# Kernel tuning notes

Measured on AMD Instinct MI355X. Metric: run time of the kernel, lower is better.

## Reference

```python
import jax, jax.numpy as jnp
import numpy as np

B, T, R, D, M = 4, 256, 100, 128, 256

def setup_inputs() -> dict:
    key = jax.random.key(0)
    ks = jax.random.split(key, 12)
    s = 0.02
    return {
        'x': jax.random.normal(ks[0], (B, T, R, D), dtype=jnp.float32),
        'mask': jax.random.randint(ks[1], (B, T), 0, 2).astype(jnp.int32),
        'Wq': jax.random.normal(ks[2], (D, D), dtype=jnp.float32) * s,
        'bq': jnp.zeros((D,), jnp.float32),
        'Wk': jax.random.normal(ks[3], (D, D), dtype=jnp.float32) * s,
        'bk': jnp.zeros((D,), jnp.float32),
        'Wv': jax.random.normal(ks[4], (D, D), dtype=jnp.float32) * s,
        'bv': jnp.zeros((D,), jnp.float32),
        'Wp': jax.random.normal(ks[5], (D, D), dtype=jnp.float32) * s,
        'bp': jnp.zeros((D,), jnp.float32),
        'ln_g': jnp.ones((D,), jnp.float32),
        'ln_b': jnp.zeros((D,), jnp.float32),
        'rel_table': jax.random.normal(ks[6], (2 * M - 1, 1), dtype=jnp.float32) * s,
    }


def reference(x, mask, Wq, bq, Wk, bk, Wv, bv, Wp, bp, ln_g, ln_b, rel_table):
    b, t, r, d = x.shape
    m = (rel_table.shape[0] + 1) // 2  # max_time_steps
    # faithful to torch .view(B*R, T, D): raw row-major reshape (no transpose)
    xr = x.reshape(b * r, t, d)
    q = xr @ Wq + bq
    k = xr @ Wk + bk
    v = xr @ Wv + bv
    scale = jnp.asarray(1.0 / np.sqrt(d), x.dtype)
    s = jnp.einsum('ntd,nsd->nts', q, k) * scale  # [B*R, T, T]
    # relative position bias
    ids = jnp.clip(jnp.arange(t)[:, None] - jnp.arange(t)[None, :] + (m - 1), 0, 2 * m - 2)
    s = s + rel_table[ids, 0][None, :, :]
    # padding mask (key and query sides)
    am = jnp.repeat(mask[:, None, :], r, axis=1).reshape(b * r, t)  # [B*R, T]
    neg = jnp.asarray(-1e9, s.dtype)
    s = jnp.where(am[:, None, :] == 0, neg, s)
    s = jnp.where(am[:, :, None] == 0, neg, s)
    # causal mask
    causal = jnp.triu(jnp.ones((t, t), dtype=bool), 1)
    s = jnp.where(causal[None, :, :], neg, s)
    w = jax.nn.softmax(s, axis=-1)
    ctx = jnp.einsum('nts,nsd->ntd', w, v)
    out = ctx @ Wp + bp
    y = xr + out
    mu = jnp.mean(y, axis=-1, keepdims=True)
    var = jnp.mean((y - mu) ** 2, axis=-1, keepdims=True)
    y = (y - mu) / jnp.sqrt(var + 1e-5) * ln_g + ln_b
    # faithful to torch .view(B, R, T, D).permute(0, 2, 1, 3)
    return y.reshape(b, r, t, d).transpose(0, 2, 1, 3)
```

## Files before the change

kernel.cpp:

```cpp
#include <hip/hip_runtime.h>
#include <hip/hip_bf16.h>
#include <stdint.h>

typedef float f32x4 __attribute__((ext_vector_type(4)));
typedef __bf16 bf16x8 __attribute__((ext_vector_type(8)));
typedef unsigned short u16;

#define MFMA16(a, b, c) __builtin_amdgcn_mfma_f32_16x16x32_bf16((a), (b), (c), 0, 0, 0)

__device__ __forceinline__ u16 f2bf(float f) {
  union { float f; uint32_t u; } v; v.f = f;
  uint32_t u = v.u;
  return (u16)((u + 0x7fffu + ((u >> 16) & 1u)) >> 16);
}
__device__ __forceinline__ float bf2f(u16 h) {
  union { uint32_t u; float f; } v; v.u = ((uint32_t)h) << 16;
  return v.f;
}

__global__ void prep_weights_kernel(const float* __restrict__ Wq, const float* __restrict__ Wk,
                                    const float* __restrict__ Wv, const float* __restrict__ Wp,
                                    u16* __restrict__ Wt) {
  int w = blockIdx.x;
  const float* W = (w == 0) ? Wq : (w == 1) ? Wk : (w == 2) ? Wv : Wp;
  int t = blockIdx.y * 256 + threadIdx.x;
  int c = t >> 7, k = t & 127;
  Wt[(w * 128 + c) * 128 + k] = f2bf(W[k * 128 + c]);
}

__global__ __launch_bounds__(512, 2) void fused11_kernel(
    const u16* __restrict__ Wt, const float* __restrict__ x,
    const int* __restrict__ mask, const float* __restrict__ rel,
    const float* __restrict__ bq, const float* __restrict__ bk,
    const float* __restrict__ bv, const float* __restrict__ bp,
    const float* __restrict__ ln_g, const float* __restrict__ ln_b,
    float* __restrict__ out) {
  __shared__ u16 KX[256][136];
  __shared__ u16 V_lds[128][264];
  __shared__ u16 P_lds[8][32][40];
  __shared__ float rel_lds[511];
  __shared__ float vmean_lds[128];
  const int tid = threadIdx.x;
  const int n = blockIdx.x;
  const int bb = n / 100, rr = n - bb * 100;
  const int* mrow = mask + bb * 256;
  if (tid < 511) rel_lds[tid] = rel[tid];
  const int l = tid & 63, wv = tid >> 6, l15 = l & 15, l4 = l >> 4;
  const int tt0 = wv * 32;

#define LOADW4(buf, ROWB)                                                  \
  do {                                                                     \
    const u16* _wp = Wt + (size_t)((ROWB) + l15) * 128 + l4 * 8;           \
    buf[0] = *(const bf16x8*)(_wp);                                        \
    buf[1] = *(const bf16x8*)(_wp + 32);                                   \
    buf[2] = *(const bf16x8*)(_wp + 64);                                   \
    buf[3] = *(const bf16x8*)(_wp + 96);                                   \
  } while (0)

  bf16x8 bA[4], bB[4];
  LOADW4(bA, 0);

  {
    int row = tt0 + (l >> 1), half = (l & 1) * 64;
    const float* src = x + ((size_t)(n * 256 + row)) * 128 + half;
    u16* dst = &KX[row][half];
    float4 xr[16];
#pragma unroll
    for (int j = 0; j < 16; ++j) xr[j] = ((const float4*)src)[j];
#pragma unroll
    for (int j = 0; j < 16; ++j) {
      dst[j * 4 + 0] = f2bf(xr[j].x); dst[j * 4 + 1] = f2bf(xr[j].y);
      dst[j * 4 + 2] = f2bf(xr[j].z); dst[j * 4 + 3] = f2bf(xr[j].w);
    }
  }
  int ttg[2][4], qm[2][4];
#pragma unroll
  for (int g = 0; g < 2; ++g)
#pragma unroll
    for (int rg = 0; rg < 4; ++rg) {
      ttg[g][rg] = tt0 + g * 16 + 4 * l4 + rg;
      qm[g][rg] = mrow[ttg[g][rg]];
    }

  bf16x8 af[2][4];
#pragma unroll
  for (int g = 0; g < 2; ++g)
#pragma unroll
    for (int ks = 0; ks < 4; ++ks)
      af[g][ks] = *(const bf16x8*)&KX[tt0 + g * 16 + l15][ks * 32 + l4 * 8];
  uint32_t xres[2][4][4];
#pragma unroll
  for (int g = 0; g < 2; ++g)
#pragma unroll
    for (int rg = 0; rg < 4; ++rg) {
      const u16* xr = &KX[tt0 + g * 16 + 4 * l4 + rg][0];
#pragma unroll
      for (int c = 0; c < 4; ++c)
        xres[g][rg][c] = (uint32_t)xr[c * 32 + l15] | ((uint32_t)xr[c * 32 + 16 + l15] << 16);
    }

  const float scale = 0.088388347648318447f;
  f32x4 t0, t1;
#define MF8(buf)                                                           \
  do {                                                                     \
    t0 = f32x4{0.f, 0.f, 0.f, 0.f}; t1 = f32x4{0.f, 0.f, 0.f, 0.f};       \
    _Pragma("unroll") for (int ks = 0; ks < 4; ++ks) {                     \
      t0 = MFMA16(af[0][ks], buf[ks], t0);                                 \
      t1 = MFMA16(af[1][ks], buf[ks], t1);                                 \
    }                                                                      \
  } while (0)

  bf16x8 qa[2][4];
#define QSTORE(CT)                                                         \
  do {                                                                     \
    float bqv = bq[(CT) * 16 + l15];                                       \
    _Pragma("unroll") for (int rg = 0; rg < 4; ++rg) {                     \
      P_lds[wv][4 * l4 + rg][((CT) & 1) * 16 + l15] = f2bf((t0[rg] + bqv) * scale); \
      P_lds[wv][16 + 4 * l4 + rg][((CT) & 1) * 16 + l15] = f2bf((t1[rg] + bqv) * scale); \
    }                                                                      \
    if ((CT) & 1) {                                                        \
      qa[0][(CT) >> 1] = *(const bf16x8*)&P_lds[wv][l15][l4 * 8];          \
      qa[1][(CT) >> 1] = *(const bf16x8*)&P_lds[wv][16 + l15][l4 * 8];     \
    }                                                                      \
  } while (0)
  LOADW4(bB, 16);
  MF8(bA); LOADW4(bA, 2 * 16);        QSTORE(0);
  MF8(bB); LOADW4(bB, 3 * 16);        QSTORE(1);
  MF8(bA); LOADW4(bA, 4 * 16);        QSTORE(2);
  MF8(bB); LOADW4(bB, 5 * 16);        QSTORE(3);
  MF8(bA); LOADW4(bA, 6 * 16);        QSTORE(4);
  MF8(bB); LOADW4(bB, 7 * 16);        QSTORE(5);
  MF8(bA); LOADW4(bA, 128 + wv * 16); QSTORE(6);
  MF8(bB); LOADW4(bB, 256 + wv * 16); QSTORE(7);

  __syncthreads();

  const float bkv = bk[wv * 16 + l15];
  const float bvv = bv[wv * 16 + l15];
  f32x4 kacc[16];
#pragma unroll
  for (int r = 0; r < 16; ++r) {
    bf16x8 xf[4];
#pragma unroll
    for (int ks = 0; ks < 4; ++ks)
      xf[ks] = *(const bf16x8*)&KX[r * 16 + l15][ks * 32 + l4 * 8];
    f32x4 ka = f32x4{0.f, 0.f, 0.f, 0.f};
    f32x4 va = f32x4{0.f, 0.f, 0.f, 0.f};
#pragma unroll
    for (int ks = 0; ks < 4; ++ks) {
      ka = MFMA16(xf[ks], bA[ks], ka);
      va = MFMA16(xf[ks], bB[ks], va);
    }
    kacc[r] = ka;
#pragma unroll
    for (int rg = 0; rg < 4; ++rg)
      V_lds[wv * 16 + l15][r * 16 + 4 * l4 + rg] = f2bf(va[rg] + bvv);
  }
  __syncthreads();
#pragma unroll
  for (int r = 0; r < 16; ++r)
#pragma unroll
    for (int rg = 0; rg < 4; ++rg)
      KX[r * 16 + 4 * l4 + rg][wv * 16 + l15] = f2bf(kacc[r][rg] + bkv);
  __syncthreads();

  {
    int d = tid >> 2, seg = tid & 3;
    const u16* vr = &V_lds[d][seg * 64];
    float s = 0.f;
#pragma unroll
    for (int j = 0; j < 8; ++j) {
      uint4 u = *(const uint4*)(vr + j * 8);
      s += bf2f((u16)(u.x & 0xffff)) + bf2f((u16)(u.x >> 16));
      s += bf2f((u16)(u.y & 0xffff)) + bf2f((u16)(u.y >> 16));
      s += bf2f((u16)(u.z & 0xffff)) + bf2f((u16)(u.z >> 16));
      s += bf2f((u16)(u.w & 0xffff)) + bf2f((u16)(u.w >> 16));
    }
    s += __shfl_xor(s, 1); s += __shfl_xor(s, 2);
    if (seg == 0) vmean_lds[d] = s * (1.f / 256.f);
  }
  float lsum[2][4]; f32x4 cacc[2][8];
#pragma unroll
  for (int g = 0; g < 2; ++g)
#pragma unroll
    for (int rg = 0; rg < 4; ++rg) lsum[g][rg] = 0.f;
#pragma unroll
  for (int g = 0; g < 2; ++g)
#pragma unroll
    for (int ct = 0; ct < 8; ++ct) cacc[g][ct] = f32x4{0.f, 0.f, 0.f, 0.f};
  __syncthreads();

  const int nkv = (wv >> 1) + 1;
  for (int kv = 0; kv < nkv; ++kv) {
    const int s0 = kv * 64;
    f32x4 sacc[2][4];
#pragma unroll
    for (int g = 0; g < 2; ++g)
#pragma unroll
      for (int ct = 0; ct < 4; ++ct) sacc[g][ct] = f32x4{0.f, 0.f, 0.f, 0.f};
#pragma unroll
    for (int ct = 0; ct < 4; ++ct)
#pragma unroll
      for (int ks = 0; ks < 4; ++ks) {
        bf16x8 bfr = *(const bf16x8*)&KX[s0 + ct * 16 + l15][ks * 32 + l4 * 8];
#pragma unroll
        for (int g = 0; g < 2; ++g) sacc[g][ct] = MFMA16(qa[g][ks], bfr, sacc[g][ct]);
      }
    int km[4];
#pragma unroll
    for (int ct = 0; ct < 4; ++ct) km[ct] = mrow[s0 + ct * 16 + l15];
    float p[2][4][4];
#pragma unroll
    for (int g = 0; g < 2; ++g)
#pragma unroll
      for (int ct = 0; ct < 4; ++ct) {
        const int ss = s0 + ct * 16 + l15;
#pragma unroll
        for (int rg = 0; rg < 4; ++rg) {
          float sv = sacc[g][ct][rg] + rel_lds[ttg[g][rg] - ss + 255];
          bool msk = (ss > ttg[g][rg]) | (km[ct] == 0) | (qm[g][rg] == 0);
          sv = msk ? -1.0e9f : sv;
          float pv = __expf(sv);
          p[g][ct][rg] = pv;
          lsum[g][rg] += pv;
        }
      }
#pragma unroll
    for (int c = 0; c < 2; ++c) {
#pragma unroll
      for (int g = 0; g < 2; ++g)
#pragma unroll
        for (int c2 = 0; c2 < 2; ++c2)
#pragma unroll
          for (int rg = 0; rg < 4; ++rg)
            P_lds[wv][g * 16 + 4 * l4 + rg][c2 * 16 + l15] = f2bf(p[g][2 * c + c2][rg]);
      bf16x8 pa[2];
#pragma unroll
      for (int g = 0; g < 2; ++g)
        pa[g] = *(const bf16x8*)&P_lds[wv][g * 16 + l15][l4 * 8];
#pragma unroll
      for (int ct = 0; ct < 8; ++ct) {
        bf16x8 vb = *(const bf16x8*)&V_lds[ct * 16 + l15][s0 + c * 32 + l4 * 8];
#pragma unroll
        for (int g = 0; g < 2; ++g) cacc[g][ct] = MFMA16(pa[g], vb, cacc[g][ct]);
      }
    }
  }
  float li[2][4];
#pragma unroll
  for (int g = 0; g < 2; ++g)
#pragma unroll
    for (int rg = 0; rg < 4; ++rg) {
      float rs = lsum[g][rg];
#pragma unroll
      for (int off = 1; off < 16; off <<= 1) rs += __shfl_xor(rs, off);
      li[g][rg] = rs;
    }
  __syncthreads();

#pragma unroll
  for (int g = 0; g < 2; ++g)
#pragma unroll
    for (int ct = 0; ct < 8; ++ct) {
      float vm = vmean_lds[ct * 16 + l15];
#pragma unroll
      for (int rg = 0; rg < 4; ++rg) {
        float cval = cacc[g][ct][rg] / li[g][rg];
        cval = (qm[g][rg] == 0) ? vm : cval;
        KX[ttg[g][rg]][ct * 16 + l15] = f2bf(cval);
      }
    }
  __syncthreads();

  u16* ybuf = (u16*)V_lds;
  LOADW4(bA, 384 + wv * 16);
  const float bpw = bp[wv * 16 + l15];
#pragma unroll
  for (int r = 0; r < 16; ++r) {
    bf16x8 cf[4];
#pragma unroll
    for (int ks = 0; ks < 4; ++ks)
      cf[ks] = *(const bf16x8*)&KX[r * 16 + l15][ks * 32 + l4 * 8];
    f32x4 ya = f32x4{0.f, 0.f, 0.f, 0.f};
#pragma unroll
    for (int ks = 0; ks < 4; ++ks) ya = MFMA16(cf[ks], bA[ks], ya);
#pragma unroll
    for (int rg = 0; rg < 4; ++rg)
      ybuf[(size_t)(r * 16 + 4 * l4 + rg) * 132 + wv * 16 + l15] = f2bf(ya[rg] + bpw);
  }
  __syncthreads();

  float gv[8], bt[8];
#pragma unroll
  for (int ct = 0; ct < 8; ++ct) {
    int d = ct * 16 + l15;
    gv[ct] = ln_g[d]; bt[ct] = ln_b[d];
  }
#pragma unroll
  for (int g = 0; g < 2; ++g)
#pragma unroll
    for (int rg = 0; rg < 4; ++rg) {
      const int tg = ttg[g][rg];
      const u16* yr = ybuf + (size_t)tg * 132;
      float yv[8], sum = 0.f, sq = 0.f;
#pragma unroll
      for (int ct = 0; ct < 8; ++ct) {
        uint32_t pr = xres[g][rg][ct >> 1];
        u16 xh = (ct & 1) ? (u16)(pr >> 16) : (u16)(pr & 0xffff);
        float v = bf2f(yr[ct * 16 + l15]) + bf2f(xh);
        yv[ct] = v; sum += v; sq += v * v;
      }
#pragma unroll
      for (int off = 1; off < 16; off <<= 1) { sum += __shfl_xor(sum, off); sq += __shfl_xor(sq, off); }
      float mean = sum * (1.f / 128.f);
      float var = sq * (1.f / 128.f) - mean * mean;
      float rstd = rsqrtf(var + 1e-5f);
      float* orow = out + (((size_t)(bb * 256 + tg)) * 100 + rr) * 128;
#pragma unroll
      for (int ct = 0; ct < 8; ++ct)
        orow[ct * 16 + l15] = (yv[ct] - mean) * rstd * gv[ct] + bt[ct];
    }
#undef LOADW4
#undef MF8
#undef QSTORE
}

extern "C" void kernel_launch(void* const* d_in, const int* in_sizes, int n_in,
                              void* d_out, int out_size, void* d_ws, size_t ws_size,
                              hipStream_t stream) {
  const float* x    = (const float*)d_in[0];
  const int*   mask = (const int*)d_in[1];
  const float* Wq   = (const float*)d_in[2];
  const float* bq   = (const float*)d_in[3];
  const float* Wk   = (const float*)d_in[4];
  const float* bk   = (const float*)d_in[5];
  const float* Wv   = (const float*)d_in[6];
  const float* bv   = (const float*)d_in[7];
  const float* Wp   = (const float*)d_in[8];
  const float* bp   = (const float*)d_in[9];
  const float* ln_g = (const float*)d_in[10];
  const float* ln_b = (const float*)d_in[11];
  const float* rel  = (const float*)d_in[12];
  float* out = (float*)d_out;
  u16* Wt = (u16*)d_ws;

  hipLaunchKernelGGL(prep_weights_kernel, dim3(4, 64), dim3(256), 0, stream, Wq, Wk, Wv, Wp, Wt);
  hipLaunchKernelGGL(fused11_kernel, dim3(400), dim3(512), 0, stream,
                     Wt, x, mask, rel, bq, bk, bv, bp, ln_g, ln_b, out);
}
```

Measured before the change: 89.15 us.

## Balance causal attention work across waves by pairing low and high query row tiles

Result: no change. 87.84 us (-1.5%).

```diff
diff --git a/kernel.cpp b/kernel.cpp
--- a/kernel.cpp
+++ b/kernel.cpp
@@ -28,7 +28,7 @@
   Wt[(w * 128 + c) * 128 + k] = f2bf(W[k * 128 + c]);
 }
 
-__global__ __launch_bounds__(512, 2) void fused11_kernel(
+__global__ __launch_bounds__(512, 2) void fused12_kernel(
     const u16* __restrict__ Wt, const float* __restrict__ x,
     const int* __restrict__ mask, const float* __restrict__ rel,
     const float* __restrict__ bq, const float* __restrict__ bk,
@@ -46,7 +46,7 @@
   const int* mrow = mask + bb * 256;
   if (tid < 511) rel_lds[tid] = rel[tid];
   const int l = tid & 63, wv = tid >> 6, l15 = l & 15, l4 = l >> 4;
-  const int tt0 = wv * 32;
+  const int rbase0 = wv * 16, rbase1 = (15 - wv) * 16;
 
 #define LOADW4(buf, ROWB)                                                  \
   do {                                                                     \
@@ -61,7 +61,8 @@
   LOADW4(bA, 0);
 
   {
-    int row = tt0 + (l >> 1), half = (l & 1) * 64;
+    int rb = (l < 32) ? rbase0 : rbase1;
+    int row = rb + ((l & 31) >> 1), half = (l & 1) * 64;
     const float* src = x + ((size_t)(n * 256 + row)) * 128 + half;
     u16* dst = &KX[row][half];
     float4 xr[16];
@@ -73,12 +74,13 @@
       dst[j * 4 + 2] = f2bf(xr[j].z); dst[j * 4 + 3] = f2bf(xr[j].w);
     }
   }
+  const int rb[2] = {rbase0, rbase1};
   int ttg[2][4], qm[2][4];
 #pragma unroll
   for (int g = 0; g < 2; ++g)
 #pragma unroll
     for (int rg = 0; rg < 4; ++rg) {
-      ttg[g][rg] = tt0 + g * 16 + 4 * l4 + rg;
+      ttg[g][rg] = rb[g] + 4 * l4 + rg;
       qm[g][rg] = mrow[ttg[g][rg]];
     }
 
@@ -87,13 +89,13 @@
   for (int g = 0; g < 2; ++g)
 #pragma unroll
     for (int ks = 0; ks < 4; ++ks)
-      af[g][ks] = *(const bf16x8*)&KX[tt0 + g * 16 + l15][ks * 32 + l4 * 8];
+      af[g][ks] = *(const bf16x8*)&KX[rb[g] + l15][ks * 32 + l4 * 8];
   uint32_t xres[2][4][4];
 #pragma unroll
   for (int g = 0; g < 2; ++g)
 #pragma unroll
     for (int rg = 0; rg < 4; ++rg) {
-      const u16* xr = &KX[tt0 + g * 16 + 4 * l4 + rg][0];
+      const u16* xr = &KX[rb[g] + 4 * l4 + rg][0];
 #pragma unroll
       for (int c = 0; c < 4; ++c)
         xres[g][rg][c] = (uint32_t)xr[c * 32 + l15] | ((uint32_t)xr[c * 32 + 16 + l15] << 16);
@@ -190,59 +192,52 @@
     for (int ct = 0; ct < 8; ++ct) cacc[g][ct] = f32x4{0.f, 0.f, 0.f, 0.f};
   __syncthreads();
 
-  const int nkv = (wv >> 1) + 1;
-  for (int kv = 0; kv < nkv; ++kv) {
-    const int s0 = kv * 64;
-    f32x4 sacc[2][4];
-#pragma unroll
-    for (int g = 0; g < 2; ++g)
-#pragma unroll
-      for (int ct = 0; ct < 4; ++ct) sacc[g][ct] = f32x4{0.f, 0.f, 0.f, 0.f};
-#pragma unroll
-    for (int ct = 0; ct < 4; ++ct)
-#pragma unroll
-      for (int ks = 0; ks < 4; ++ks) {
-        bf16x8 bfr = *(const bf16x8*)&KX[s0 + ct * 16 + l15][ks * 32 + l4 * 8];
-#pragma unroll
-        for (int g = 0; g < 2; ++g) sacc[g][ct] = MFMA16(qa[g][ks], bfr, sacc[g][ct]);
-      }
-    int km[4];
-#pragma unroll
-    for (int ct = 0; ct < 4; ++ct) km[ct] = mrow[s0 + ct * 16 + l15];
-    float p[2][4][4];
-#pragma unroll
-    for (int g = 0; g < 2; ++g)
+#pragma unroll
+  for (int g = 0; g < 2; ++g) {
+    const int nkvg = (rb[g] >> 6) + 1;
+#pragma unroll 1
+    for (int kv = 0; kv < nkvg; ++kv) {
+      const int s0 = kv * 64;
+      f32x4 sacc[4];
+#pragma unroll
+      for (int ct = 0; ct < 4; ++ct) sacc[ct] = f32x4{0.f, 0.f, 0.f, 0.f};
+#pragma unroll
+      for (int ct = 0; ct < 4; ++ct)
+#pragma unroll
+        for (int ks = 0; ks < 4; ++ks) {
+          bf16x8 bfr = *(const bf16x8*)&KX[s0 + ct * 16 + l15][ks * 32 + l4 * 8];
+          sacc[ct] = MFMA16(qa[g][ks], bfr, sacc[ct]);
+        }
+      int km[4];
+#pragma unroll
+      for (int ct = 0; ct < 4; ++ct) km[ct] = mrow[s0 + ct * 16 + l15];
+      float p[4][4];
 #pragma unroll
       for (int ct = 0; ct < 4; ++ct) {
         const int ss = s0 + ct * 16 + l15;
 #pragma unroll
         for (int rg = 0; rg < 4; ++rg) {
-          float sv = sacc[g][ct][rg] + rel_lds[ttg[g][rg] - ss + 255];
+          float sv = sacc[ct][rg] + rel_lds[ttg[g][rg] - ss + 255];
           bool msk = (ss > ttg[g][rg]) | (km[ct] == 0) | (qm[g][rg] == 0);
           sv = msk ? -1.0e9f : sv;
           float pv = __expf(sv);
-          p[g][ct][rg] = pv;
+          p[ct][rg] = pv;
           lsum[g][rg] += pv;
         }
       }
 #pragma unroll
-    for (int c = 0; c < 2; ++c) {
-#pragma unroll
-      for (int g = 0; g < 2; ++g)
+      for (int c = 0; c < 2; ++c) {
 #pragma unroll
         for (int c2 = 0; c2 < 2; ++c2)
 #pragma unroll
           for (int rg = 0; rg < 4; ++rg)
-            P_lds[wv][g * 16 + 4 * l4 + rg][c2 * 16 + l15] = f2bf(p[g][2 * c + c2][rg]);
-      bf16x8 pa[2];
-#pragma unroll
-      for (int g = 0; g < 2; ++g)
-        pa[g] = *(const bf16x8*)&P_lds[wv][g * 16 + l15][l4 * 8];
-#pragma unroll
-      for (int ct = 0; ct < 8; ++ct) {
-        bf16x8 vb = *(const bf16x8*)&V_lds[ct * 16 + l15][s0 + c * 32 + l4 * 8];
-#pragma unroll
-        for (int g = 0; g < 2; ++g) cacc[g][ct] = MFMA16(pa[g], vb, cacc[g][ct]);
+            P_lds[wv][g * 16 + 4 * l4 + rg][c2 * 16 + l15] = f2bf(p[2 * c + c2][rg]);
+        bf16x8 pa = *(const bf16x8*)&P_lds[wv][g * 16 + l15][l4 * 8];
+#pragma unroll
+        for (int ct = 0; ct < 8; ++ct) {
+          bf16x8 vb = *(const bf16x8*)&V_lds[ct * 16 + l15][s0 + c * 32 + l4 * 8];
+          cacc[g][ct] = MFMA16(pa, vb, cacc[g][ct]);
+        }
       }
     }
   }
@@ -345,6 +340,6 @@
   u16* Wt = (u16*)d_ws;
 
   hipLaunchKernelGGL(prep_weights_kernel, dim3(4, 64), dim3(256), 0, stream, Wq, Wk, Wv, Wp, Wt);
-  hipLaunchKernelGGL(fused11_kernel, dim3(400), dim3(512), 0, stream,
+  hipLaunchKernelGGL(fused12_kernel, dim3(400), dim3(512), 0, stream,
                      Wt, x, mask, rel, bq, bk, bv, bp, ln_g, ln_b, out);
 }
```
